# Kernel tuning notes

Measured on AMD Instinct MI355X. Metric: run time of the kernel, lower is better.

Reference implementation:

```python
import jax, jax.numpy as jnp
import numpy as np

N = 100000     # total nodes in batch
E = 1600000    # total edges in batch
G = 1024       # number of graphs in batch
IN, H1, H2, FC, OUT = 128, 128, 128, 128, 1


def setup_inputs() -> dict:
    key = jax.random.key(0)
    ks = jax.random.split(key, 8)
    node_feats = jax.random.normal(ks[0], (N, IN), jnp.float32)
    adj = jax.random.randint(ks[1], (2, E), 0, N)
    graph_idx = jnp.sort(jax.random.randint(ks[2], (N,), 0, G))
    init = lambda k, sh, fan: jax.random.normal(k, sh, jnp.float32) / np.float32(np.sqrt(fan))
    W1 = init(ks[3], (IN, H1), IN); b1 = jnp.zeros((H1,), jnp.float32)
    W2 = init(ks[4], (H1, H2), H1); b2 = jnp.zeros((H2,), jnp.float32)
    Wfc = init(ks[5], (H2, FC), H2); bfc = jnp.zeros((FC,), jnp.float32)
    Wout = init(ks[6], (FC, OUT), FC); bout = jnp.zeros((OUT,), jnp.float32)
    return dict(node_feats=node_feats, adj=adj, graph_idx=graph_idx, is_training=0,
                W1=W1, b1=b1, W2=W2, b2=b2, Wfc=Wfc, bfc=bfc, Wout=Wout, bout=bout)


def _gcn_layer(x, src, dst, W, b):
    # h = relu( D^{-1/2} A D^{-1/2} (x W + b) ), A given as an edge list (src -> dst)
    h = x @ W + b                                   # [N, H]
    ones = jnp.ones((src.shape[0],), h.dtype)
    deg = jax.ops.segment_sum(ones, dst, num_segments=N)      # node degrees
    norm = jnp.where(deg > 0, jax.lax.rsqrt(jnp.maximum(deg, 1.0)), 0.0)
    msg = h[src] * norm[src][:, None]               # gather over edges [E, H]
    agg = jax.ops.segment_sum(msg, dst, num_segments=N) * norm[:, None]
    return jax.nn.relu(agg)


def reference(node_feats, adj, graph_idx, is_training, W1, b1, W2, b2, Wfc, bfc, Wout, bout):
    src, dst = adj[0], adj[1]
    h = _gcn_layer(node_feats, src, dst, W1, b1)
    h = _gcn_layer(h, src, dst, W2, b2)
    # mean pooling per graph (segment mean)
    counts = jax.ops.segment_sum(jnp.ones((N,), h.dtype), graph_idx, num_segments=G)
    graph_feat = jax.ops.segment_sum(h, graph_idx, num_segments=G) / jnp.maximum(counts, 1.0)[:, None]
    # MLP head (predicator_dropout = 0.0, is_training=False -> no dropout)
    graph_feat = jax.nn.relu(graph_feat @ Wfc + bfc)
    return graph_feat @ Wout + bout                 # [G, n_out]
```

## Files before the change

kernel.cpp:

```cpp
#include <hip/hip_runtime.h>


typedef unsigned short ushort_t;
typedef unsigned int   uint_t;
typedef unsigned char  uchar_t;
typedef __attribute__((ext_vector_type(8))) short bf16x8;
typedef __attribute__((ext_vector_type(4))) float f32x4;
typedef __attribute__((ext_vector_type(2))) float f32x2;

#define EPB     4096
#define CAP2    32
#define BKT_CAP 8192

__device__ __forceinline__ float bf2f(uint_t u) { return __uint_as_float(u << 16); }
__device__ __forceinline__ ushort_t f2bf(float f) {
  uint_t x = __float_as_uint(f);
  x = x + 0x7fffu + ((x >> 16) & 1u);
  return (ushort_t)(x >> 16);
}

__device__ __forceinline__ bf16x8 pack8(float4 u, float4 v) {
  union { uint4 q; bf16x8 b; } cv;
  cv.q.x = (uint_t)f2bf(u.x) | ((uint_t)f2bf(u.y) << 16);
  cv.q.y = (uint_t)f2bf(u.z) | ((uint_t)f2bf(u.w) << 16);
  cv.q.z = (uint_t)f2bf(v.x) | ((uint_t)f2bf(v.y) << 16);
  cv.q.w = (uint_t)f2bf(v.z) | ((uint_t)f2bf(v.w) << 16);
  return cv.b;
}

__global__ __launch_bounds__(256, 4) void k_front(const float* __restrict__ X, const float* __restrict__ W1,
                                                  const float* __restrict__ b1, uchar_t* __restrict__ Yf8,
                                                  const float* __restrict__ W2, ushort_t* __restrict__ Wf2,
                                                  const int* __restrict__ src, const int* __restrict__ dst,
                                                  uint_t* __restrict__ binbuf, int* __restrict__ cntmatT,
                                                  int E, int N, int nblk, int nbkt, int GB1) {
  __shared__ ushort_t Ws[16384];
  __shared__ int cur[512];
  int t = threadIdx.x;
  int bid = blockIdx.x;

  if (bid < nblk) {
    for (int r = t; r < nbkt; r += 256) cur[r] = 0;
    __syncthreads();
    int base = bid * EPB;
#pragma unroll
    for (int j = 0; j < EPB / 256; j++) {
      int e = base + j * 256 + t;
      if (e < E) {
        int s = src[e], d = dst[e];
        int b = d >> 8;
        int p = atomicAdd(&cur[b], 1);
        if (p < CAP2)
          binbuf[((size_t)b * nblk + bid) * CAP2 + p] = (uint_t)s | ((uint_t)(d & 255) << 17);
      }
    }
    __syncthreads();
    for (int r = t; r < nbkt; r += 256) {
      int c = cur[r];
      cntmatT[(size_t)r * nblk + bid] = (c < CAP2) ? c : CAP2;
    }
    return;
  }
  if (bid < nblk + 64) {
    if (bid == nblk && t < 8) ((uint4*)Yf8)[(size_t)N * 8 + t] = make_uint4(0u, 0u, 0u, 0u);
    int idx = (bid - nblk) * 256 + t;
    int n = idx & 127, k = idx >> 7;
    Wf2[((size_t)(k >> 3) * 128 + n) * 8 + (k & 7)] = f2bf(W2[(size_t)k * 128 + n]);
    return;
  }

  {
    const float4* W4 = (const float4*)W1;
#pragma unroll
    for (int i = 0; i < 16; i++) {
      int idx = i * 256 + t;
      int k = idx >> 5;
      int n0 = (idx & 31) * 4;
      float4 v = W4[idx];
      int qb = k >> 3, j = k & 7;
      Ws[((size_t)qb * 128 + n0 + 0) * 8 + j] = f2bf(v.x);
      Ws[((size_t)qb * 128 + n0 + 1) * 8 + j] = f2bf(v.y);
      Ws[((size_t)qb * 128 + n0 + 2) * 8 + j] = f2bf(v.z);
      Ws[((size_t)qb * 128 + n0 + 3) * 8 + j] = f2bf(v.w);
    }
  }
  int r0 = (bid - nblk - 64) * 128;
  int wave = t >> 6, lane = t & 63;
  int ln = lane & 15, quad = lane >> 4;
  int row0 = r0 + wave * 32 + ln;
  int row1 = row0 + 16;
  int cr0 = min(row0, N - 1);
  int cr1 = min(row1, N - 1);

  bf16x8 a0[4], a1[4];
  {
    const float4* Xp = (const float4*)X;
#pragma unroll
    for (int kc = 0; kc < 4; kc++) {
      int q = kc * 4 + quad;
      float4 u0 = Xp[(size_t)cr0 * 32 + q * 2];
      float4 v0 = Xp[(size_t)cr0 * 32 + q * 2 + 1];
      float4 u1 = Xp[(size_t)cr1 * 32 + q * 2];
      float4 v1 = Xp[(size_t)cr1 * 32 + q * 2 + 1];
      a0[kc] = pack8(u0, v0);
      a1[kc] = pack8(u1, v1);
    }
  }
  __syncthreads();

  const bf16x8* Wb = (const bf16x8*)Ws;
  f32x4 acc[2][8];
#pragma unroll
  for (int mt = 0; mt < 2; mt++)
#pragma unroll
    for (int ct = 0; ct < 8; ct++) acc[mt][ct] = (f32x4){0.f, 0.f, 0.f, 0.f};

#pragma unroll
  for (int kc = 0; kc < 4; kc++) {
    int q = kc * 4 + quad;
#pragma unroll
    for (int ct = 0; ct < 8; ct++) {
      bf16x8 b = Wb[q * 128 + ct * 16 + ln];
      acc[0][ct] = __builtin_amdgcn_mfma_f32_16x16x32_bf16(b, a0[kc], acc[0][ct], 0, 0, 0);
      acc[1][ct] = __builtin_amdgcn_mfma_f32_16x16x32_bf16(b, a1[kc], acc[1][ct], 0, 0, 0);
    }
  }

  int chbase = quad * 4;
  float4 bs[8];
#pragma unroll
  for (int ct = 0; ct < 8; ct++) bs[ct] = *(const float4*)(b1 + ct * 16 + chbase);
  uint_t* Y32 = (uint_t*)Yf8;
  if (row0 < N) {
#pragma unroll
    for (int ct = 0; ct < 8; ct++) {
      f32x4 v = acc[0][ct];
      float x0 = (v[0] + bs[ct].x) * 16.f, x1 = (v[1] + bs[ct].y) * 16.f;
      float x2 = (v[2] + bs[ct].z) * 16.f, x3 = (v[3] + bs[ct].w) * 16.f;
      int w = __builtin_amdgcn_cvt_pk_fp8_f32(x0, x1, 0, false);
      w = __builtin_amdgcn_cvt_pk_fp8_f32(x2, x3, w, true);
      Y32[(size_t)row0 * 32 + ct * 4 + quad] = (uint_t)w;
    }
  }
  if (row1 < N) {
#pragma unroll
    for (int ct = 0; ct < 8; ct++) {
      f32x4 v = acc[1][ct];
      float x0 = (v[0] + bs[ct].x) * 16.f, x1 = (v[1] + bs[ct].y) * 16.f;
      float x2 = (v[2] + bs[ct].z) * 16.f, x3 = (v[3] + bs[ct].w) * 16.f;
      int w = __builtin_amdgcn_cvt_pk_fp8_f32(x0, x1, 0, false);
      w = __builtin_amdgcn_cvt_pk_fp8_f32(x2, x3, w, true);
      Y32[(size_t)row1 * 32 + ct * 4 + quad] = (uint_t)w;
    }
  }
}

__global__ __launch_bounds__(512) void k_csr(const uint_t* __restrict__ binbuf, const int* __restrict__ cntmatT,
                                             int* __restrict__ esrc, int* __restrict__ deg,
                                             int* __restrict__ offs, float* __restrict__ nrm,
                                             int N, int nblk) {
  __shared__ int cnt_s[512];
  __shared__ int hist[256];
  __shared__ int cur[256];
  __shared__ int wsum[4];
  __shared__ int lsrc[BKT_CAP];
  int b = blockIdx.x, t = threadIdx.x;
  if (b == 0 && t == 0) nrm[N] = 0.f;
  int n0 = b << 8;
  int gbase = b * BKT_CAP;
  for (int r = t; r < nblk; r += 512) cnt_s[r] = cntmatT[(size_t)b * nblk + r];
  if (t < 256) hist[t] = 0;
  __syncthreads();
  const uint4* seg4 = (const uint4*)(binbuf + (size_t)b * nblk * CAP2);
  int total4 = (nblk * CAP2) >> 2;
  for (int i4 = t; i4 < total4; i4 += 512) {
    int base = i4 << 2;
    int c = cnt_s[base >> 5];
    int s0 = base & 31;
    if (s0 < c) {
      uint4 v = seg4[i4];
      int nv = c - s0;
      atomicAdd(&hist[v.x >> 17], 1);
      if (nv > 1) atomicAdd(&hist[v.y >> 17], 1);
      if (nv > 2) atomicAdd(&hist[v.z >> 17], 1);
      if (nv > 3) atomicAdd(&hist[v.w >> 17], 1);
    }
  }
  __syncthreads();
  int lane = t & 63, wv = t >> 6;
  if (t < 256) {
    int h = hist[t];
    int incl = h;
#pragma unroll
    for (int s = 1; s < 64; s <<= 1) {
      int x = __shfl_up(incl, s, 64);
      if (lane >= s) incl += x;
    }
    if (lane == 63) wsum[wv] = incl;
    __syncthreads();
    int wbase = 0;
#pragma unroll
    for (int k = 0; k < 4; k++) wbase += (k < wv) ? wsum[k] : 0;
    int excl = wbase + incl - h;
    cur[t] = excl;
    int node = n0 + t;
    if (node < N) {
      deg[node] = h;
      offs[node] = gbase + excl;
      nrm[node] = (h > 0) ? rsqrtf((float)h) : 0.f;
    }
  } else {
    __syncthreads();
  }
  __syncthreads();
  int count = wsum[0] + wsum[1] + wsum[2] + wsum[3];
  for (int i4 = t; i4 < total4; i4 += 512) {
    int base = i4 << 2;
    int c = cnt_s[base >> 5];
    int s0 = base & 31;
    if (s0 < c) {
      uint4 v = seg4[i4];
      int nv = c - s0;
      { int p = atomicAdd(&cur[v.x >> 17], 1); lsrc[p] = (int)(v.x & 0x1ffffu); }
      if (nv > 1) { int p = atomicAdd(&cur[v.y >> 17], 1); lsrc[p] = (int)(v.y & 0x1ffffu); }
      if (nv > 2) { int p = atomicAdd(&cur[v.z >> 17], 1); lsrc[p] = (int)(v.z & 0x1ffffu); }
      if (nv > 3) { int p = atomicAdd(&cur[v.w >> 17], 1); lsrc[p] = (int)(v.w & 0x1ffffu); }
    }
  }
  __syncthreads();
  for (int i = t; i < count; i += 512) esrc[gbase + i] = lsrc[i];
}

__global__ __launch_bounds__(256, 4) void k_gemm2(const ushort_t* __restrict__ Xb, const ushort_t* __restrict__ Wf,
                                                  const float* __restrict__ bias, const float* __restrict__ nrm,
                                                  uchar_t* __restrict__ Yf8, int nrows) {
  __shared__ ushort_t Ws[16384];
  int tid = threadIdx.x;
  int r0 = blockIdx.x * 128;
  {
    const uint4* s = (const uint4*)Wf;
    uint4* d = (uint4*)Ws;
#pragma unroll
    for (int i = 0; i < 8; i++) d[tid + 256 * i] = s[tid + 256 * i];
  }
  int wave = tid >> 6, lane = tid & 63;
  int ln = lane & 15, quad = lane >> 4;
  int row0 = r0 + wave * 32 + ln;
  int row1 = row0 + 16;
  int cr0 = min(row0, nrows - 1);
  int cr1 = min(row1, nrows - 1);

  bf16x8 a0[4], a1[4];
  {
    const uint4* Xp = (const uint4*)Xb;
#pragma unroll
    for (int kc = 0; kc < 4; kc++) {
      int q = kc * 4 + quad;
      union { uint4 u; bf16x8 b; } c0, c1;
      c0.u = Xp[(size_t)cr0 * 16 + q];
      c1.u = Xp[(size_t)cr1 * 16 + q];
      a0[kc] = c0.b;
      a1[kc] = c1.b;
    }
  }
  __syncthreads();

  const bf16x8* Wb = (const bf16x8*)Ws;
  f32x4 acc[2][8];
#pragma unroll
  for (int mt = 0; mt < 2; mt++)
#pragma unroll
    for (int ct = 0; ct < 8; ct++) acc[mt][ct] = (f32x4){0.f, 0.f, 0.f, 0.f};

#pragma unroll
  for (int kc = 0; kc < 4; kc++) {
    int q = kc * 4 + quad;
#pragma unroll
    for (int ct = 0; ct < 8; ct++) {
      bf16x8 b = Wb[q * 128 + ct * 16 + ln];
      acc[0][ct] = __builtin_amdgcn_mfma_f32_16x16x32_bf16(b, a0[kc], acc[0][ct], 0, 0, 0);
      acc[1][ct] = __builtin_amdgcn_mfma_f32_16x16x32_bf16(b, a1[kc], acc[1][ct], 0, 0, 0);
    }
  }

  int chbase = quad * 4;
  float4 bs[8];
#pragma unroll
  for (int ct = 0; ct < 8; ct++) bs[ct] = *(const float4*)(bias + ct * 16 + chbase);
  float nv0 = nrm[cr0] * 16.f;
  float nv1 = nrm[cr1] * 16.f;
  uint_t* Y32 = (uint_t*)Yf8;
  if (row0 < nrows) {
#pragma unroll
    for (int ct = 0; ct < 8; ct++) {
      f32x4 v = acc[0][ct];
      float x0 = (v[0] + bs[ct].x) * nv0, x1 = (v[1] + bs[ct].y) * nv0;
      float x2 = (v[2] + bs[ct].z) * nv0, x3 = (v[3] + bs[ct].w) * nv0;
      int w = __builtin_amdgcn_cvt_pk_fp8_f32(x0, x1, 0, false);
      w = __builtin_amdgcn_cvt_pk_fp8_f32(x2, x3, w, true);
      Y32[(size_t)row0 * 32 + ct * 4 + quad] = (uint_t)w;
    }
  }
  if (row1 < nrows) {
#pragma unroll
    for (int ct = 0; ct < 8; ct++) {
      f32x4 v = acc[1][ct];
      float x0 = (v[0] + bs[ct].x) * nv1, x1 = (v[1] + bs[ct].y) * nv1;
      float x2 = (v[2] + bs[ct].z) * nv1, x3 = (v[3] + bs[ct].w) * nv1;
      int w = __builtin_amdgcn_cvt_pk_fp8_f32(x0, x1, 0, false);
      w = __builtin_amdgcn_cvt_pk_fp8_f32(x2, x3, w, true);
      Y32[(size_t)row1 * 32 + ct * 4 + quad] = (uint_t)w;
    }
  }
}

__device__ __forceinline__ void acc16p(f32x2* a, uint4 g) {
  a[0] += __builtin_amdgcn_cvt_pk_f32_fp8((int)g.x, false);
  a[1] += __builtin_amdgcn_cvt_pk_f32_fp8((int)g.x, true);
  a[2] += __builtin_amdgcn_cvt_pk_f32_fp8((int)g.y, false);
  a[3] += __builtin_amdgcn_cvt_pk_f32_fp8((int)g.y, true);
  a[4] += __builtin_amdgcn_cvt_pk_f32_fp8((int)g.z, false);
  a[5] += __builtin_amdgcn_cvt_pk_f32_fp8((int)g.z, true);
  a[6] += __builtin_amdgcn_cvt_pk_f32_fp8((int)g.w, false);
  a[7] += __builtin_amdgcn_cvt_pk_f32_fp8((int)g.w, true);
}

__device__ __forceinline__ void acc16f(f32x2* a, uint4 g, float s) {
  f32x2 sv = {s, s};
  a[0] += __builtin_amdgcn_cvt_pk_f32_fp8((int)g.x, false) * sv;
  a[1] += __builtin_amdgcn_cvt_pk_f32_fp8((int)g.x, true)  * sv;
  a[2] += __builtin_amdgcn_cvt_pk_f32_fp8((int)g.y, false) * sv;
  a[3] += __builtin_amdgcn_cvt_pk_f32_fp8((int)g.y, true)  * sv;
  a[4] += __builtin_amdgcn_cvt_pk_f32_fp8((int)g.z, false) * sv;
  a[5] += __builtin_amdgcn_cvt_pk_f32_fp8((int)g.z, true)  * sv;
  a[6] += __builtin_amdgcn_cvt_pk_f32_fp8((int)g.w, false) * sv;
  a[7] += __builtin_amdgcn_cvt_pk_f32_fp8((int)g.w, true)  * sv;
}

__device__ __forceinline__ uint_t pk2(f32x2 v, float nv) {
  float a = fmaxf(v.x * nv, 0.f);
  float b = fmaxf(v.y * nv, 0.f);
  return (uint_t)f2bf(a) | ((uint_t)f2bf(b) << 16);
}

template <bool EDGE_NRM>
__global__ __launch_bounds__(256) void k_agg(const uint4* __restrict__ hn8, const int* __restrict__ offs,
                                             const int* __restrict__ deg, const float* __restrict__ nrm,
                                             const int* __restrict__ esrc, uint4* __restrict__ outb, int N) {
  int wave = threadIdx.x >> 6, lane = threadIdx.x & 63;
  int sub = lane >> 3, sl = lane & 7;
  int node = blockIdx.x * 32 + wave * 8 + sub;
  bool live = node < N;
  int d  = live ? deg[node] : 0;
  int eb = live ? offs[node] : 0;
  int maxd = d;
  maxd = max(maxd, __shfl_xor(maxd, 8, 64));
  maxd = max(maxd, __shfl_xor(maxd, 16, 64));
  maxd = max(maxd, __shfl_xor(maxd, 32, 64));
  f32x2 A[8] = {};
  f32x2 B[8] = {};
  int it = 0;
  for (; it + 4 <= maxd; it += 4) {
    int x0 = esrc[eb + it];
    int x1 = esrc[eb + it + 1];
    int x2 = esrc[eb + it + 2];
    int x3 = esrc[eb + it + 3];
    x0 = (it < d) ? x0 : N;
    x1 = (it + 1 < d) ? x1 : N;
    x2 = (it + 2 < d) ? x2 : N;
    x3 = (it + 3 < d) ? x3 : N;
    uint4 g0 = hn8[(size_t)x0 * 8 + sl];
    uint4 g1 = hn8[(size_t)x1 * 8 + sl];
    uint4 g2 = hn8[(size_t)x2 * 8 + sl];
    uint4 g3 = hn8[(size_t)x3 * 8 + sl];
    if (EDGE_NRM) {
      float s0 = nrm[x0], s1 = nrm[x1], s2 = nrm[x2], s3 = nrm[x3];
      acc16f(A, g0, s0); acc16f(B, g1, s1);
      acc16f(A, g2, s2); acc16f(B, g3, s3);
    } else {
      acc16p(A, g0); acc16p(B, g1);
      acc16p(A, g2); acc16p(B, g3);
    }
  }
  for (; it < maxd; it += 2) {
    int x0 = esrc[eb + it];
    int x1 = esrc[eb + it + 1];
    x0 = (it < d) ? x0 : N;
    x1 = (it + 1 < d) ? x1 : N;
    uint4 g0 = hn8[(size_t)x0 * 8 + sl];
    uint4 g1 = hn8[(size_t)x1 * 8 + sl];
    if (EDGE_NRM) {
      float s0 = nrm[x0], s1 = nrm[x1];
      acc16f(A, g0, s0); acc16f(B, g1, s1);
    } else {
      acc16p(A, g0); acc16p(B, g1);
    }
  }
  if (!live) return;
  float nv = nrm[node] * 0.0625f;
  uint4 p0, p1;
  p0.x = pk2(A[0] + B[0], nv); p0.y = pk2(A[1] + B[1], nv);
  p0.z = pk2(A[2] + B[2], nv); p0.w = pk2(A[3] + B[3], nv);
  p1.x = pk2(A[4] + B[4], nv); p1.y = pk2(A[5] + B[5], nv);
  p1.z = pk2(A[6] + B[6], nv); p1.w = pk2(A[7] + B[7], nv);
  outb[(size_t)node * 16 + sl * 2]     = p0;
  outb[(size_t)node * 16 + sl * 2 + 1] = p1;
}

__device__ __forceinline__ int lowerb(const int* __restrict__ a, int n, int v) {
  int lo = 0, hi = n;
  while (lo < hi) { int m = (lo + hi) >> 1; if (a[m] < v) lo = m + 1; else hi = m; }
  return lo;
}

__global__ __launch_bounds__(256) void k_head(const ushort_t* __restrict__ h2, const int* __restrict__ gidx,
                                              const float* __restrict__ Wfc, const float* __restrict__ bfc,
                                              const float* __restrict__ Wout, const float* __restrict__ bout,
                                              float* __restrict__ out, int N) {
  __shared__ float partial[4][128];
  __shared__ float pv[128];
  __shared__ float fcp[2][128];
  __shared__ float red[128];
  __shared__ int segb[2];
  int g = blockIdx.x, t = threadIdx.x;
  int wave = t >> 6, lane = t & 63;
  if (t == 0)  segb[0] = lowerb(gidx, N, g);
  if (t == 64) segb[1] = lowerb(gidx, N, g + 1);
  __syncthreads();
  int lo = segb[0], hi = segb[1];
  int q = lane & 15;
  int r4 = lane >> 4;
  const uint4* h4 = (const uint4*)h2;
  f32x2 A[4] = {};
  for (int i = lo + wave * 4 + r4; i < hi; i += 16) {
    uint4 v = h4[(size_t)i * 16 + q];
    A[0] += (f32x2){__uint_as_float(v.x << 16), __uint_as_float(v.x & 0xffff0000u)};
    A[1] += (f32x2){__uint_as_float(v.y << 16), __uint_as_float(v.y & 0xffff0000u)};
    A[2] += (f32x2){__uint_as_float(v.z << 16), __uint_as_float(v.z & 0xffff0000u)};
    A[3] += (f32x2){__uint_as_float(v.w << 16), __uint_as_float(v.w & 0xffff0000u)};
  }
#pragma unroll
  for (int k = 0; k < 4; k++) {
    A[k].x += __shfl_xor(A[k].x, 16, 64); A[k].y += __shfl_xor(A[k].y, 16, 64);
    A[k].x += __shfl_xor(A[k].x, 32, 64); A[k].y += __shfl_xor(A[k].y, 32, 64);
  }
  if (lane < 16) {
    partial[wave][q * 8 + 0] = A[0].x; partial[wave][q * 8 + 1] = A[0].y;
    partial[wave][q * 8 + 2] = A[1].x; partial[wave][q * 8 + 3] = A[1].y;
    partial[wave][q * 8 + 4] = A[2].x; partial[wave][q * 8 + 5] = A[2].y;
    partial[wave][q * 8 + 6] = A[3].x; partial[wave][q * 8 + 7] = A[3].y;
  }
  __syncthreads();
  if (t < 128) {
    float c = (float)(hi - lo); if (c < 1.f) c = 1.f;
    float s = (partial[0][t] + partial[1][t]) + (partial[2][t] + partial[3][t]);
    pv[t] = s / c;
  }
  __syncthreads();
  int col = t & 127, half = t >> 7;
  float acc = (half == 0) ? bfc[col] : 0.f;
  const float* Wc = Wfc + (size_t)half * 64 * 128 + col;
#pragma unroll 8
  for (int k = 0; k < 64; k++) acc += pv[half * 64 + k] * Wc[k * 128];
  fcp[half][col] = acc;
  __syncthreads();
  if (t < 128) {
    float a = fmaxf(fcp[0][t] + fcp[1][t], 0.f);
    red[t] = a * Wout[t];
  }
  __syncthreads();
  if (t < 64) {
    float v2 = red[t] + red[t + 64];
#pragma unroll
    for (int s = 32; s > 0; s >>= 1) v2 += __shfl_xor(v2, s, 64);
    if (t == 0) out[g] = v2 + bout[0];
  }
}


extern "C" void kernel_launch(void* const* d_in, const int* in_sizes, int n_in,
                              void* d_out, int out_size, void* d_ws, size_t ws_size,
                              hipStream_t stream) {
  const float* X    = (const float*)d_in[0];
  const int*   adj  = (const int*)d_in[1];
  const int*   gidx = (const int*)d_in[2];
  const float* W1   = (const float*)d_in[4];
  const float* b1   = (const float*)d_in[5];
  const float* W2   = (const float*)d_in[6];
  const float* b2   = (const float*)d_in[7];
  const float* Wfc  = (const float*)d_in[8];
  const float* bfc  = (const float*)d_in[9];
  const float* Wout = (const float*)d_in[10];
  const float* bout = (const float*)d_in[11];
  (void)n_in; (void)ws_size;

  const int N = in_sizes[2];
  const int E = in_sizes[1] / 2;
  const int G = out_size;
  const int* srcv = adj;
  const int* dstv = adj + E;
  const int nbkt = (N + 255) >> 8;
  const int nblk = (E + EPB - 1) / EPB;
  const int GB1  = (N + 127) / 128;

  char* w = (char*)d_ws;
  size_t off = 0;
  auto alloc = [&](size_t bytes) -> void* {
    void* p = (void*)(w + off);
    off += (bytes + 255) & ~(size_t)255;
    return p;
  };
  uchar_t*  bufA  = (uchar_t*)alloc((size_t)(N + 1) * 128);
  ushort_t* bufB  = (ushort_t*)alloc((size_t)N * 128 * sizeof(ushort_t));
  float*    nrm   = (float*)alloc((size_t)(N + 1) * sizeof(float));
  int*      deg   = (int*)alloc((size_t)N * sizeof(int));
  int*      offs  = (int*)alloc((size_t)N * sizeof(int));
  int*      esrc  = (int*)alloc(((size_t)nbkt * BKT_CAP + BKT_CAP) * sizeof(int));
  uint_t*   binb  = (uint_t*)alloc((size_t)nbkt * nblk * CAP2 * sizeof(uint_t));
  int*      cmatT = (int*)alloc((size_t)nbkt * nblk * sizeof(int));
  ushort_t* Wf2   = (ushort_t*)alloc((size_t)128 * 128 * sizeof(ushort_t));

  k_front<<<nblk + 64 + GB1, 256, 0, stream>>>(X, W1, b1, bufA, W2, Wf2,
                                               srcv, dstv, binb, cmatT,
                                               E, N, nblk, nbkt, GB1);
  k_csr<<<nbkt, 512, 0, stream>>>(binb, cmatT, esrc, deg, offs, nrm, N, nblk);

  const int aggGrid = (N + 31) / 32;
  k_agg<true><<<aggGrid, 256, 0, stream>>>((const uint4*)bufA, offs, deg, nrm, esrc, (uint4*)bufB, N);
  k_gemm2<<<GB1, 256, 0, stream>>>(bufB, Wf2, b2, nrm, bufA, N);
  k_agg<false><<<aggGrid, 256, 0, stream>>>((const uint4*)bufA, offs, deg, nrm, esrc, (uint4*)bufB, N);
  k_head<<<G, 256, 0, stream>>>(bufB, gidx, Wfc, bfc, Wout, bout, (float*)d_out, N);
}
```

Measured before the change: 253.2 us.

## Fuse first-layer aggregation with second-layer GEMM into one kernel

The layer-1 edge aggregation is merged with the layer-2 dense transform. Each 32-node block stages its aggregated bf16 rows in shared memory, then runs MFMA against W2 read from global memory and writes fp8 output to a new separate buffer. This removes the bf16 intermediate round trip through global memory and one kernel launch. In exchange, each block now reads all of W2 from global or cache instead of staging it once in LDS per 128 rows, and the aggregation tail gets a barrier and lower occupancy.

```diff
diff --git a/kernel.cpp b/kernel.cpp
--- a/kernel.cpp
+++ b/kernel.cpp
@@ -30,6 +30,7 @@
 
 __global__ __launch_bounds__(256, 4) void k_front(const float* __restrict__ X, const float* __restrict__ W1,
                                                   const float* __restrict__ b1, uchar_t* __restrict__ Yf8,
+                                                  uchar_t* __restrict__ YfC,
                                                   const float* __restrict__ W2, ushort_t* __restrict__ Wf2,
                                                   const int* __restrict__ src, const int* __restrict__ dst,
                                                   uint_t* __restrict__ binbuf, int* __restrict__ cntmatT,
@@ -62,7 +63,9 @@
     return;
   }
   if (bid < nblk + 64) {
-    if (bid == nblk && t < 8) ((uint4*)Yf8)[(size_t)N * 8 + t] = make_uint4(0u, 0u, 0u, 0u);
+    if (bid == nblk && t < 8)  ((uint4*)Yf8)[(size_t)N * 8 + t] = make_uint4(0u, 0u, 0u, 0u);
+    if (bid == nblk && t >= 8 && t < 16)
+      ((uint4*)YfC)[(size_t)N * 8 + (t - 8)] = make_uint4(0u, 0u, 0u, 0u);
     int idx = (bid - nblk) * 256 + t;
     int n = idx & 127, k = idx >> 7;
     Wf2[((size_t)(k >> 3) * 128 + n) * 8 + (k & 7)] = f2bf(W2[(size_t)k * 128 + n]);
@@ -231,89 +234,6 @@
   for (int i = t; i < count; i += 512) esrc[gbase + i] = lsrc[i];
 }
 
-__global__ __launch_bounds__(256, 4) void k_gemm2(const ushort_t* __restrict__ Xb, const ushort_t* __restrict__ Wf,
-                                                  const float* __restrict__ bias, const float* __restrict__ nrm,
-                                                  uchar_t* __restrict__ Yf8, int nrows) {
-  __shared__ ushort_t Ws[16384];
-  int tid = threadIdx.x;
-  int r0 = blockIdx.x * 128;
-  {
-    const uint4* s = (const uint4*)Wf;
-    uint4* d = (uint4*)Ws;
-#pragma unroll
-    for (int i = 0; i < 8; i++) d[tid + 256 * i] = s[tid + 256 * i];
-  }
-  int wave = tid >> 6, lane = tid & 63;
-  int ln = lane & 15, quad = lane >> 4;
-  int row0 = r0 + wave * 32 + ln;
-  int row1 = row0 + 16;
-  int cr0 = min(row0, nrows - 1);
-  int cr1 = min(row1, nrows - 1);
-
-  bf16x8 a0[4], a1[4];
-  {
-    const uint4* Xp = (const uint4*)Xb;
-#pragma unroll
-    for (int kc = 0; kc < 4; kc++) {
-      int q = kc * 4 + quad;
-      union { uint4 u; bf16x8 b; } c0, c1;
-      c0.u = Xp[(size_t)cr0 * 16 + q];
-      c1.u = Xp[(size_t)cr1 * 16 + q];
-      a0[kc] = c0.b;
-      a1[kc] = c1.b;
-    }
-  }
-  __syncthreads();
-
-  const bf16x8* Wb = (const bf16x8*)Ws;
-  f32x4 acc[2][8];
-#pragma unroll
-  for (int mt = 0; mt < 2; mt++)
-#pragma unroll
-    for (int ct = 0; ct < 8; ct++) acc[mt][ct] = (f32x4){0.f, 0.f, 0.f, 0.f};
-
-#pragma unroll
-  for (int kc = 0; kc < 4; kc++) {
-    int q = kc * 4 + quad;
-#pragma unroll
-    for (int ct = 0; ct < 8; ct++) {
-      bf16x8 b = Wb[q * 128 + ct * 16 + ln];
-      acc[0][ct] = __builtin_amdgcn_mfma_f32_16x16x32_bf16(b, a0[kc], acc[0][ct], 0, 0, 0);
-      acc[1][ct] = __builtin_amdgcn_mfma_f32_16x16x32_bf16(b, a1[kc], acc[1][ct], 0, 0, 0);
-    }
-  }
-
-  int chbase = quad * 4;
-  float4 bs[8];
-#pragma unroll
-  for (int ct = 0; ct < 8; ct++) bs[ct] = *(const float4*)(bias + ct * 16 + chbase);
-  float nv0 = nrm[cr0] * 16.f;
-  float nv1 = nrm[cr1] * 16.f;
-  uint_t* Y32 = (uint_t*)Yf8;
-  if (row0 < nrows) {
-#pragma unroll
-    for (int ct = 0; ct < 8; ct++) {
-      f32x4 v = acc[0][ct];
-      float x0 = (v[0] + bs[ct].x) * nv0, x1 = (v[1] + bs[ct].y) * nv0;
-      float x2 = (v[2] + bs[ct].z) * nv0, x3 = (v[3] + bs[ct].w) * nv0;
-      int w = __builtin_amdgcn_cvt_pk_fp8_f32(x0, x1, 0, false);
-      w = __builtin_amdgcn_cvt_pk_fp8_f32(x2, x3, w, true);
-      Y32[(size_t)row0 * 32 + ct * 4 + quad] = (uint_t)w;
-    }
-  }
-  if (row1 < nrows) {
-#pragma unroll
-    for (int ct = 0; ct < 8; ct++) {
-      f32x4 v = acc[1][ct];
-      float x0 = (v[0] + bs[ct].x) * nv1, x1 = (v[1] + bs[ct].y) * nv1;
-      float x2 = (v[2] + bs[ct].z) * nv1, x3 = (v[3] + bs[ct].w) * nv1;
-      int w = __builtin_amdgcn_cvt_pk_fp8_f32(x0, x1, 0, false);
-      w = __builtin_amdgcn_cvt_pk_fp8_f32(x2, x3, w, true);
-      Y32[(size_t)row1 * 32 + ct * 4 + quad] = (uint_t)w;
-    }
-  }
-}
-
 __device__ __forceinline__ void acc16p(f32x2* a, uint4 g) {
   a[0] += __builtin_amdgcn_cvt_pk_f32_fp8((int)g.x, false);
   a[1] += __builtin_amdgcn_cvt_pk_f32_fp8((int)g.x, true);
@@ -324,7 +244,6 @@
   a[6] += __builtin_amdgcn_cvt_pk_f32_fp8((int)g.w, false);
   a[7] += __builtin_amdgcn_cvt_pk_f32_fp8((int)g.w, true);
 }
-
 __device__ __forceinline__ void acc16f(f32x2* a, uint4 g, float s) {
   f32x2 sv = {s, s};
   a[0] += __builtin_amdgcn_cvt_pk_f32_fp8((int)g.x, false) * sv;
@@ -336,17 +255,113 @@
   a[6] += __builtin_amdgcn_cvt_pk_f32_fp8((int)g.w, false) * sv;
   a[7] += __builtin_amdgcn_cvt_pk_f32_fp8((int)g.w, true)  * sv;
 }
-
 __device__ __forceinline__ uint_t pk2(f32x2 v, float nv) {
   float a = fmaxf(v.x * nv, 0.f);
   float b = fmaxf(v.y * nv, 0.f);
   return (uint_t)f2bf(a) | ((uint_t)f2bf(b) << 16);
 }
 
-template <bool EDGE_NRM>
-__global__ __launch_bounds__(256) void k_agg(const uint4* __restrict__ hn8, const int* __restrict__ offs,
-                                             const int* __restrict__ deg, const float* __restrict__ nrm,
-                                             const int* __restrict__ esrc, uint4* __restrict__ outb, int N) {
+__global__ __launch_bounds__(256, 5) void k_aggemm(const uint4* __restrict__ hn8, const int* __restrict__ offs,
+                                                   const int* __restrict__ deg, const float* __restrict__ nrm,
+                                                   const int* __restrict__ esrc, const ushort_t* __restrict__ Wf2,
+                                                   const float* __restrict__ b2, uchar_t* __restrict__ YfC,
+                                                   int N) {
+  __shared__ uint4 Hs[32 * 17];
+  int wave = threadIdx.x >> 6, lane = threadIdx.x & 63;
+  int sub = lane >> 3, sl = lane & 7;
+  int base = blockIdx.x * 32;
+  int node = base + wave * 8 + sub;
+  bool live = node < N;
+  int d  = live ? deg[node] : 0;
+  int eb = live ? offs[node] : 0;
+  int maxd = d;
+  maxd = max(maxd, __shfl_xor(maxd, 8, 64));
+  maxd = max(maxd, __shfl_xor(maxd, 16, 64));
+  maxd = max(maxd, __shfl_xor(maxd, 32, 64));
+  f32x2 A[8] = {};
+  f32x2 B[8] = {};
+  int it = 0;
+  for (; it + 4 <= maxd; it += 4) {
+    int x0 = esrc[eb + it];
+    int x1 = esrc[eb + it + 1];
+    int x2 = esrc[eb + it + 2];
+    int x3 = esrc[eb + it + 3];
+    x0 = (it < d) ? x0 : N;
+    x1 = (it + 1 < d) ? x1 : N;
+    x2 = (it + 2 < d) ? x2 : N;
+    x3 = (it + 3 < d) ? x3 : N;
+    uint4 g0 = hn8[(size_t)x0 * 8 + sl];
+    uint4 g1 = hn8[(size_t)x1 * 8 + sl];
+    uint4 g2 = hn8[(size_t)x2 * 8 + sl];
+    uint4 g3 = hn8[(size_t)x3 * 8 + sl];
+    float s0 = nrm[x0], s1 = nrm[x1], s2 = nrm[x2], s3 = nrm[x3];
+    acc16f(A, g0, s0); acc16f(B, g1, s1);
+    acc16f(A, g2, s2); acc16f(B, g3, s3);
+  }
+  for (; it < maxd; it += 2) {
+    int x0 = esrc[eb + it];
+    int x1 = esrc[eb + it + 1];
+    x0 = (it < d) ? x0 : N;
+    x1 = (it + 1 < d) ? x1 : N;
+    uint4 g0 = hn8[(size_t)x0 * 8 + sl];
+    uint4 g1 = hn8[(size_t)x1 * 8 + sl];
+    float s0 = nrm[x0], s1 = nrm[x1];
+    acc16f(A, g0, s0); acc16f(B, g1, s1);
+  }
+  float nv = nrm[live ? node : N] * 0.0625f;
+  uint4 p0, p1;
+  p0.x = pk2(A[0] + B[0], nv); p0.y = pk2(A[1] + B[1], nv);
+  p0.z = pk2(A[2] + B[2], nv); p0.w = pk2(A[3] + B[3], nv);
+  p1.x = pk2(A[4] + B[4], nv); p1.y = pk2(A[5] + B[5], nv);
+  p1.z = pk2(A[6] + B[6], nv); p1.w = pk2(A[7] + B[7], nv);
+  int lrow = wave * 8 + sub;
+  Hs[lrow * 17 + sl * 2]     = p0;
+  Hs[lrow * 17 + sl * 2 + 1] = p1;
+  __syncthreads();
+
+  int ln = lane & 15, quad = lane >> 4;
+  const bf16x8* Wb = (const bf16x8*)Wf2;
+  f32x4 acc[2][2];
+#pragma unroll
+  for (int mt = 0; mt < 2; mt++)
+#pragma unroll
+    for (int c = 0; c < 2; c++) acc[mt][c] = (f32x4){0.f, 0.f, 0.f, 0.f};
+#pragma unroll
+  for (int kc = 0; kc < 4; kc++) {
+    int q = kc * 4 + quad;
+    union { uint4 u; bf16x8 b; } a0, a1;
+    a0.u = Hs[ln * 17 + q];
+    a1.u = Hs[(16 + ln) * 17 + q];
+    bf16x8 b0 = Wb[q * 128 + (wave * 2 + 0) * 16 + ln];
+    bf16x8 b1 = Wb[q * 128 + (wave * 2 + 1) * 16 + ln];
+    acc[0][0] = __builtin_amdgcn_mfma_f32_16x16x32_bf16(b0, a0.b, acc[0][0], 0, 0, 0);
+    acc[1][0] = __builtin_amdgcn_mfma_f32_16x16x32_bf16(b0, a1.b, acc[1][0], 0, 0, 0);
+    acc[0][1] = __builtin_amdgcn_mfma_f32_16x16x32_bf16(b1, a0.b, acc[0][1], 0, 0, 0);
+    acc[1][1] = __builtin_amdgcn_mfma_f32_16x16x32_bf16(b1, a1.b, acc[1][1], 0, 0, 0);
+  }
+  uint_t* Y32 = (uint_t*)YfC;
+#pragma unroll
+  for (int mt = 0; mt < 2; mt++) {
+    int row = base + mt * 16 + ln;
+    int crw = min(row, N);
+    float nvr = nrm[crw] * 16.f;
+#pragma unroll
+    for (int c = 0; c < 2; c++) {
+      int ct = wave * 2 + c;
+      float4 bs = *(const float4*)(b2 + ct * 16 + quad * 4);
+      f32x4 v = acc[mt][c];
+      float x0 = (v[0] + bs.x) * nvr, x1 = (v[1] + bs.y) * nvr;
+      float x2 = (v[2] + bs.z) * nvr, x3 = (v[3] + bs.w) * nvr;
+      int w = __builtin_amdgcn_cvt_pk_fp8_f32(x0, x1, 0, false);
+      w = __builtin_amdgcn_cvt_pk_fp8_f32(x2, x3, w, true);
+      if (row < N) Y32[(size_t)row * 32 + ct * 4 + quad] = (uint_t)w;
+    }
+  }
+}
+
+__global__ __launch_bounds__(256) void k_agg2(const uint4* __restrict__ hn8, const int* __restrict__ offs,
+                                              const int* __restrict__ deg, const float* __restrict__ nrm,
+                                              const int* __restrict__ esrc, uint4* __restrict__ outb, int N) {
   int wave = threadIdx.x >> 6, lane = threadIdx.x & 63;
   int sub = lane >> 3, sl = lane & 7;
   int node = blockIdx.x * 32 + wave * 8 + sub;
@@ -373,14 +388,8 @@
     uint4 g1 = hn8[(size_t)x1 * 8 + sl];
     uint4 g2 = hn8[(size_t)x2 * 8 + sl];
     uint4 g3 = hn8[(size_t)x3 * 8 + sl];
-    if (EDGE_NRM) {
-      float s0 = nrm[x0], s1 = nrm[x1], s2 = nrm[x2], s3 = nrm[x3];
-      acc16f(A, g0, s0); acc16f(B, g1, s1);
-      acc16f(A, g2, s2); acc16f(B, g3, s3);
-    } else {
-      acc16p(A, g0); acc16p(B, g1);
-      acc16p(A, g2); acc16p(B, g3);
-    }
+    acc16p(A, g0); acc16p(B, g1);
+    acc16p(A, g2); acc16p(B, g3);
   }
   for (; it < maxd; it += 2) {
     int x0 = esrc[eb + it];
@@ -389,12 +398,7 @@
     x1 = (it + 1 < d) ? x1 : N;
     uint4 g0 = hn8[(size_t)x0 * 8 + sl];
     uint4 g1 = hn8[(size_t)x1 * 8 + sl];
-    if (EDGE_NRM) {
-      float s0 = nrm[x0], s1 = nrm[x1];
-      acc16f(A, g0, s0); acc16f(B, g1, s1);
-    } else {
-      acc16p(A, g0); acc16p(B, g1);
-    }
+    acc16p(A, g0); acc16p(B, g1);
   }
   if (!live) return;
   float nv = nrm[node] * 0.0625f;
@@ -511,6 +515,7 @@
     return p;
   };
   uchar_t*  bufA  = (uchar_t*)alloc((size_t)(N + 1) * 128);
+  uchar_t*  bufC  = (uchar_t*)alloc((size_t)(N + 1) * 128);
   ushort_t* bufB  = (ushort_t*)alloc((size_t)N * 128 * sizeof(ushort_t));
   float*    nrm   = (float*)alloc((size_t)(N + 1) * sizeof(float));
   int*      deg   = (int*)alloc((size_t)N * sizeof(int));
@@ -520,14 +525,14 @@
   int*      cmatT = (int*)alloc((size_t)nbkt * nblk * sizeof(int));
   ushort_t* Wf2   = (ushort_t*)alloc((size_t)128 * 128 * sizeof(ushort_t));
 
-  k_front<<<nblk + 64 + GB1, 256, 0, stream>>>(X, W1, b1, bufA, W2, Wf2,
+  k_front<<<nblk + 64 + GB1, 256, 0, stream>>>(X, W1, b1, bufA, bufC, W2, Wf2,
                                                srcv, dstv, binb, cmatT,
                                                E, N, nblk, nbkt, GB1);
   k_csr<<<nbkt, 512, 0, stream>>>(binb, cmatT, esrc, deg, offs, nrm, N, nblk);
 
   const int aggGrid = (N + 31) / 32;
-  k_agg<true><<<aggGrid, 256, 0, stream>>>((const uint4*)bufA, offs, deg, nrm, esrc, (uint4*)bufB, N);
-  k_gemm2<<<GB1, 256, 0, stream>>>(bufB, Wf2, b2, nrm, bufA, N);
-  k_agg<false><<<aggGrid, 256, 0, stream>>>((const uint4*)bufA, offs, deg, nrm, esrc, (uint4*)bufB, N);
+  k_aggemm<<<aggGrid, 256, 0, stream>>>((const uint4*)bufA, offs, deg, nrm, esrc,
+                                        Wf2, b2, bufC, N);
+  k_agg2<<<aggGrid, 256, 0, stream>>>((const uint4*)bufC, offs, deg, nrm, esrc, (uint4*)bufB, N);
   k_head<<<G, 256, 0, stream>>>(bufB, gidx, Wfc, bfc, Wout, bout, (float*)d_out, N);
 }
```

After: 246.6 us. 1.03x faster.
